# Kernel tuning notes

Hardware: AMD Instinct MI355X
Metric: run time of the kernel (lower is better)

## Reference

```python
import jax, jax.numpy as jnp
import numpy as np

N = 32768      # total nodes (2048 graphs * 16 nodes)
E = 491520     # total edges (2048 graphs * 16*15)
F = 11         # in_node_nf
H = 64         # hidden_nf
G = 2048       # number of graphs
NN = 16        # nodes per graph
R = 1024       # n_reactions
L = 4          # n_layers
EIN = 2 * H + 1        # edge_mlp input: [h[row], h[col], radial]
NIN = H + H + F        # node_mlp input: [h, agg, node_attr=h0]


def setup_inputs() -> dict:
    key = jax.random.key(0)
    ks = jax.random.split(key, 24)
    s = 0.05
    d = {
        "h0": jax.random.normal(ks[0], (N, F), jnp.float32),
        "positions": jax.random.normal(ks[1], (N, 3), jnp.float32),
        "edges": jax.random.randint(ks[2], (2, E), 0, N),
        "node_mask": jnp.ones((N, 1), jnp.float32),
        "edge_mask": jnp.ones((E, 1), jnp.float32),
        "reaction_indexes": jax.random.randint(ks[3], (G,), 0, R),
        "reaction_signs": jax.random.normal(ks[4], (G,), jnp.float32),
        # params
        "emb_w": jax.random.normal(ks[5], (F, H), jnp.float32) * s,
        "emb_b": jnp.zeros((H,), jnp.float32),
        "edge_w1": jax.random.normal(ks[6], (L, EIN, H), jnp.float32) * s,
        "edge_b1": jnp.zeros((L, H), jnp.float32),
        "edge_w2": jax.random.normal(ks[7], (L, H, H), jnp.float32) * s,
        "edge_b2": jnp.zeros((L, H), jnp.float32),
        "node_w1": jax.random.normal(ks[8], (L, NIN, H), jnp.float32) * s,
        "node_b1": jnp.zeros((L, H), jnp.float32),
        "node_w2": jax.random.normal(ks[9], (L, H, H), jnp.float32) * s,
        "node_b2": jnp.zeros((L, H), jnp.float32),
        "dec_w1": jax.random.normal(ks[10], (H, H), jnp.float32) * s,
        "dec_b1": jnp.zeros((H,), jnp.float32),
        "dec_w2": jax.random.normal(ks[11], (H, H), jnp.float32) * s,
        "dec_b2": jnp.zeros((H,), jnp.float32),
        "g_w1": jax.random.normal(ks[12], (H, H), jnp.float32) * s,
        "g_b1": jnp.zeros((H,), jnp.float32),
        "g_w2": jax.random.normal(ks[13], (H, 1), jnp.float32) * s,
        "g_b2": jnp.zeros((1,), jnp.float32),
        "n_nodes": NN,
        "n_reactions": R,
    }
    return d


def reference(h0, positions, edges, node_mask, edge_mask, reaction_indexes,
              reaction_signs, emb_w, emb_b, edge_w1, edge_b1, edge_w2, edge_b2,
              node_w1, node_b1, node_w2, node_b2, dec_w1, dec_b1, dec_w2,
              dec_b2, g_w1, g_b1, g_w2, g_b2, n_nodes, n_reactions):
    silu = jax.nn.silu
    row, col = edges[0], edges[1]
    n = h0.shape[0]

    # radial is constant across layers (coords never updated in this variant)
    coord_diff = positions[row] - positions[col]          # [E, 3]
    radial = jnp.sum(coord_diff ** 2, axis=1, keepdims=True)  # [E, 1]

    h = h0 @ emb_w + emb_b                                # [N, H]
    for i in range(edge_w1.shape[0]):
        # edge model
        e_in = jnp.concatenate([h[row], h[col], radial], axis=1)  # [E, 2H+1]
        e = silu(e_in @ edge_w1[i] + edge_b1[i])
        e = silu(e @ edge_w2[i] + edge_b2[i])             # [E, H]
        e = e * edge_mask
        # scatter-sum aggregation by source node
        agg = jax.ops.segment_sum(e, row, num_segments=n)  # [N, H]
        # node model (node_attr = h0)
        n_in = jnp.concatenate([h, agg, h0], axis=1)      # [N, 2H+F]
        h = silu(n_in @ node_w1[i] + node_b1[i]) @ node_w2[i] + node_b2[i]

    # node decoder
    h = silu(h @ dec_w1 + dec_b1) @ dec_w2 + dec_b2
    h = h * node_mask
    # pool per graph (fixed n_nodes per graph)
    hg = h.reshape(-1, n_nodes, h.shape[-1]).sum(axis=1)  # [G, H]
    # graph decoder
    temp = silu(hg @ g_w1 + g_b1) @ g_w2 + g_b2           # [G, 1]
    # signed per-reaction aggregation
    pred = jnp.zeros((n_reactions,), h.dtype).at[reaction_indexes].add(
        temp[:, 0] * reaction_signs)
    return pred
```

## Files before the change

### kernel.cpp

```cpp
#include <hip/hip_runtime.h>
#include <math.h>

#define N_NODES 32768
#define N_EDGES 491520
#define F_IN    11
#define H       64
#define G_GRAPHS 2048
#define NN_PER_G 16
#define R_REACT 1024
#define L_LAYERS 4
#define EIN     129
#define NIN     139
#define NPBLK   32

typedef __attribute__((ext_vector_type(8))) short short8;
typedef __attribute__((ext_vector_type(4))) float f32x4;

__device__ __forceinline__ float silu_f(float x) {
    return x * __builtin_amdgcn_rcpf(1.0f + __expf(-x));
}
__device__ __forceinline__ void atomAddF(float* p, float v) {
    unsafeAtomicAdd(p, v);
}
__device__ __forceinline__ float bf2f(unsigned short b) {
    union { float f; unsigned u; } v; v.u = ((unsigned)b) << 16;
    return v.f;
}
__device__ __forceinline__ unsigned short f2bf(float x) {
    union { float f; unsigned u; } v; v.f = x;
    unsigned r = v.u + 0x7FFFu + ((v.u >> 16) & 1u);
    return (unsigned short)(r >> 16);
}
__device__ __forceinline__ void splitbf(float x, unsigned short& hi, unsigned short& lo) {
    hi = f2bf(x);
    lo = f2bf(x - bf2f(hi));
}
__device__ __forceinline__ void splitbf_t(float x, unsigned short& hi, unsigned short& lo) {
    union { float f; unsigned u; } v; v.f = x;
    hi = (unsigned short)(v.u >> 16);
    union { float f; unsigned u; } w; w.f = x - bf2f(hi);
    lo = (unsigned short)(w.u >> 16);
}

__global__ __launch_bounds__(256) void k_embed(
        const float* __restrict__ h0, const float* __restrict__ emb_w,
        const float* __restrict__ emb_b, float* __restrict__ h) {
    int tid = blockIdx.x * 256 + threadIdx.x;
    int n = tid >> 6, j = tid & 63;
    float acc = emb_b[j];
#pragma unroll
    for (int k = 0; k < F_IN; ++k)
        acc += h0[n * F_IN + k] * emb_w[k * H + j];
    h[tid] = acc;
}

__global__ __launch_bounds__(256) void k_radial(
        const int* __restrict__ edges, const float* __restrict__ pos,
        float* __restrict__ radial) {
    int e = blockIdx.x * 256 + threadIdx.x;
    int r = edges[e], c = edges[N_EDGES + e];
    float dx = pos[r * 3 + 0] - pos[c * 3 + 0];
    float dy = pos[r * 3 + 1] - pos[c * 3 + 1];
    float dz = pos[r * 3 + 2] - pos[c * 3 + 2];
    radial[e] = dx * dx + dy * dy + dz * dz;
}

__global__ __launch_bounds__(256) void k_hist(
        const int* __restrict__ edges, int* __restrict__ deg) {
    int e = blockIdx.x * 256 + threadIdx.x;
    atomicAdd(&deg[edges[e]], 1);
}

__global__ __launch_bounds__(128) void k_scan_blk(
        const int* __restrict__ deg, int* __restrict__ off,
        int* __restrict__ bsum) {
    __shared__ int sd[128];
    int b = blockIdx.x;
    sd[threadIdx.x] = deg[b * 128 + threadIdx.x];
    __syncthreads();
    if (threadIdx.x == 0) {
        int s = 0;
        for (int i = 0; i < 128; ++i) { int d = sd[i]; sd[i] = s; s += d; }
        bsum[b] = s;
    }
    __syncthreads();
    off[b * 128 + threadIdx.x] = sd[threadIdx.x];
}

__global__ __launch_bounds__(256) void k_scan_top(
        const int* __restrict__ bsum, int* __restrict__ bbase) {
    __shared__ int sb[256];
    sb[threadIdx.x] = bsum[threadIdx.x];
    __syncthreads();
    if (threadIdx.x == 0) {
        int s = 0;
        for (int i = 0; i < 256; ++i) { int d = sb[i]; sb[i] = s; s += d; }
    }
    __syncthreads();
    bbase[threadIdx.x] = sb[threadIdx.x];
}

__global__ __launch_bounds__(256) void k_cursor(
        const int* __restrict__ off, const int* __restrict__ bbase,
        int* __restrict__ nstart, int* __restrict__ cursor) {
    int n = blockIdx.x * 256 + threadIdx.x;
    int ns = off[n] + bbase[n >> 7];
    nstart[n] = ns;
    cursor[n] = ns;
    if (n == 0) nstart[N_NODES] = N_EDGES;
}

__global__ __launch_bounds__(256) void k_fill(
        const int* __restrict__ edges, const float* __restrict__ radial,
        const float* __restrict__ emask, int* __restrict__ cursor,
        int* __restrict__ csrP, float* __restrict__ csrR,
        float* __restrict__ csrM) {
    int e = blockIdx.x * 256 + threadIdx.x;
    int r = edges[e];
    int pos = atomicAdd(&cursor[r], 1);
    csrP[pos] = edges[N_EDGES + e] | ((r & (NPBLK - 1)) << 16);
    csrR[pos] = radial[e];
    csrM[pos] = emask[e];
}

__global__ __launch_bounds__(64, 1) void k_nodeproj_m(
        const float* __restrict__ h, const float* __restrict__ W1,
        const float* __restrict__ b1,
        float* __restrict__ PA, float* __restrict__ PB) {
    const int lane = threadIdx.x;
    const int quad = lane >> 4, m16 = lane & 15;

    short8 Bh[16], Bl[16];
#pragma unroll
    for (int nt = 0; nt < 8; ++nt) {
#pragma unroll
        for (int kf = 0; kf < 2; ++kf) {
            short8 bh, bl;
#pragma unroll
            for (int j = 0; j < 8; ++j) {
                int row = (nt >= 4 ? 64 : 0) + kf * 32 + quad * 8 + j;
                float w = W1[row * H + (nt & 3) * 16 + m16];
                unsigned short hi, lo; splitbf(w, hi, lo);
                bh[j] = (short)hi; bl[j] = (short)lo;
            }
            Bh[nt * 2 + kf] = bh; Bl[nt * 2 + kf] = bl;
        }
    }
    float b1v[4];
#pragma unroll
    for (int nt = 0; nt < 4; ++nt) b1v[nt] = b1[nt * 16 + m16];

    for (int t = 0; t < 2; ++t) {
        const int nb = (blockIdx.x * 2 + t) * 16;
        const float* hp = h + (nb + m16) * H + quad * 8;
        float av[16];
        *(float4*)&av[0]  = *(const float4*)(hp + 0);
        *(float4*)&av[4]  = *(const float4*)(hp + 4);
        *(float4*)&av[8]  = *(const float4*)(hp + 32);
        *(float4*)&av[12] = *(const float4*)(hp + 36);
        short8 Ah0, Ah1, Al0, Al1;
#pragma unroll
        for (int j = 0; j < 8; ++j) {
            unsigned short hi, lo;
            splitbf_t(av[j], hi, lo);     Ah0[j] = (short)hi; Al0[j] = (short)lo;
            splitbf_t(av[8 + j], hi, lo); Ah1[j] = (short)hi; Al1[j] = (short)lo;
        }
        f32x4 acc[8];
#pragma unroll
        for (int nt = 0; nt < 8; ++nt) {
            f32x4 a = {0.0f, 0.0f, 0.0f, 0.0f};
            a = __builtin_amdgcn_mfma_f32_16x16x32_bf16(Ah0, Bh[nt*2+0], a, 0, 0, 0);
            a = __builtin_amdgcn_mfma_f32_16x16x32_bf16(Ah1, Bh[nt*2+1], a, 0, 0, 0);
            a = __builtin_amdgcn_mfma_f32_16x16x32_bf16(Ah0, Bl[nt*2+0], a, 0, 0, 0);
            a = __builtin_amdgcn_mfma_f32_16x16x32_bf16(Ah1, Bl[nt*2+1], a, 0, 0, 0);
            a = __builtin_amdgcn_mfma_f32_16x16x32_bf16(Al0, Bh[nt*2+0], a, 0, 0, 0);
            a = __builtin_amdgcn_mfma_f32_16x16x32_bf16(Al1, Bh[nt*2+1], a, 0, 0, 0);
            acc[nt] = a;
        }
#pragma unroll
        for (int r4 = 0; r4 < 4; ++r4) {
            const int node = nb + quad * 4 + r4;
#pragma unroll
            for (int nt = 0; nt < 4; ++nt)
                PA[node * H + nt * 16 + m16] = acc[nt][r4] + b1v[nt];
#pragma unroll
            for (int nt = 4; nt < 8; ++nt)
                PB[node * H + (nt - 4) * 16 + m16] = acc[nt][r4];
        }
    }
}

__global__ __launch_bounds__(256, 2) void k_edge6(
        const float* __restrict__ PA, const float* __restrict__ PB,
        const int* __restrict__ nstart, const int* __restrict__ csrP,
        const float* __restrict__ csrR, const float* __restrict__ csrM,
        const float* __restrict__ W1,
        const float* __restrict__ W2, const float* __restrict__ b2,
        float* __restrict__ agg) {
    const int tid = threadIdx.x;
    const int lane = tid & 63, wave = tid >> 6;
    const int quad = lane >> 4, m16 = lane & 15;
    const int n0 = blockIdx.x * NPBLK;

    __shared__ float aggld[NPBLK * 68];
    for (int i = tid; i < NPBLK * 68; i += 256) aggld[i] = 0.0f;

    short8 Bh[8], Bl[8];
#pragma unroll
    for (int nt = 0; nt < 4; ++nt) {
#pragma unroll
        for (int kf = 0; kf < 2; ++kf) {
            short8 bh, bl;
#pragma unroll
            for (int j = 0; j < 8; ++j) {
                float w = W2[(kf * 32 + quad * 8 + j) * H + nt * 16 + m16];
                unsigned short hi, lo; splitbf(w, hi, lo);
                bh[j] = (short)hi; bl[j] = (short)lo;
            }
            Bh[nt * 2 + kf] = bh; Bl[nt * 2 + kf] = bl;
        }
    }
    float w1cr[16];
#pragma unroll
    for (int i = 0; i < 16; ++i) {
        int k = (i < 8) ? (quad * 8 + i) : (32 + quad * 8 + (i - 8));
        w1cr[i] = W1[128 * H + k];
    }
    float b2v[4];
#pragma unroll
    for (int nt = 0; nt < 4; ++nt) b2v[nt] = b2[nt * 16 + m16];

    const int start = nstart[n0];
    const int end   = nstart[n0 + NPBLK];
    __syncthreads();

    const int ntiles = (end - start + 15) >> 4;

    float radA = 0.0f, avA[16], bvA[16];
    int rlA = 0;
    int rlqA[4]; float mkqA[4];

    int t = wave;
    bool haveA = t < ntiles;
    if (haveA) {
        const int idx = start + t * 16 + m16;
        const int ss = min(idx, N_EDGES - 1);
        const int pk = csrP[ss];
        radA = csrR[ss];
        const int c = pk & 0xFFFF;
        rlA = pk >> 16;
        const int sb = start + t * 16 + quad * 4;
#pragma unroll
        for (int r4 = 0; r4 < 4; ++r4) {
            int s = sb + r4, s2 = min(s, N_EDGES - 1);
            rlqA[r4] = csrP[s2] >> 16;
            mkqA[r4] = (s < end) ? csrM[s2] : 0.0f;
        }
        const float* par = PA + (n0 + rlA) * H + quad * 8;
        const float* pbr = PB + c * H + quad * 8;
        *(float4*)&avA[0]  = *(const float4*)(par + 0);
        *(float4*)&avA[4]  = *(const float4*)(par + 4);
        *(float4*)&avA[8]  = *(const float4*)(par + 32);
        *(float4*)&avA[12] = *(const float4*)(par + 36);
        *(float4*)&bvA[0]  = *(const float4*)(pbr + 0);
        *(float4*)&bvA[4]  = *(const float4*)(pbr + 4);
        *(float4*)&bvA[8]  = *(const float4*)(pbr + 32);
        *(float4*)&bvA[12] = *(const float4*)(pbr + 36);
    }

    while (haveA) {
        const int tn = t + 4;
        const bool haveB = tn < ntiles;
        float radB = 0.0f, bvB[16];
        int rlB = 0;
        int rlqB[4]; float mkqB[4];
        if (haveB) {
            const int idx = start + tn * 16 + m16;
            const int ss = min(idx, N_EDGES - 1);
            const int pk = csrP[ss];
            radB = csrR[ss];
            const int c = pk & 0xFFFF;
            rlB = pk >> 16;
            const int sb = start + tn * 16 + quad * 4;
#pragma unroll
            for (int r4 = 0; r4 < 4; ++r4) {
                int s = sb + r4, s2 = min(s, N_EDGES - 1);
                rlqB[r4] = csrP[s2] >> 16;
                mkqB[r4] = (s < end) ? csrM[s2] : 0.0f;
            }
            const float* pbr = PB + c * H + quad * 8;
            *(float4*)&bvB[0]  = *(const float4*)(pbr + 0);
            *(float4*)&bvB[4]  = *(const float4*)(pbr + 4);
            *(float4*)&bvB[8]  = *(const float4*)(pbr + 32);
            *(float4*)&bvB[12] = *(const float4*)(pbr + 36);
        }

        short8 Ah0, Ah1, Al0, Al1;
#pragma unroll
        for (int i = 0; i < 8; ++i) {
            unsigned short hi, lo;
            splitbf_t(silu_f(avA[i] + bvA[i] + radA * w1cr[i]), hi, lo);
            Ah0[i] = (short)hi; Al0[i] = (short)lo;
            splitbf_t(silu_f(avA[8+i] + bvA[8+i] + radA * w1cr[8+i]), hi, lo);
            Ah1[i] = (short)hi; Al1[i] = (short)lo;
        }
        f32x4 acc[4];
#pragma unroll
        for (int nt = 0; nt < 4; ++nt) {
            f32x4 a = {0.0f, 0.0f, 0.0f, 0.0f};
            a = __builtin_amdgcn_mfma_f32_16x16x32_bf16(Ah0, Bh[nt*2+0], a, 0, 0, 0);
            a = __builtin_amdgcn_mfma_f32_16x16x32_bf16(Ah1, Bh[nt*2+1], a, 0, 0, 0);
            a = __builtin_amdgcn_mfma_f32_16x16x32_bf16(Ah0, Bl[nt*2+0], a, 0, 0, 0);
            a = __builtin_amdgcn_mfma_f32_16x16x32_bf16(Ah1, Bl[nt*2+1], a, 0, 0, 0);
            a = __builtin_amdgcn_mfma_f32_16x16x32_bf16(Al0, Bh[nt*2+0], a, 0, 0, 0);
            a = __builtin_amdgcn_mfma_f32_16x16x32_bf16(Al1, Bh[nt*2+1], a, 0, 0, 0);
            acc[nt] = a;
        }

#pragma unroll
        for (int nt = 0; nt < 4; ++nt) {
            float oo[4];
#pragma unroll
            for (int r4 = 0; r4 < 4; ++r4)
                oo[r4] = silu_f(acc[nt][r4] + b2v[nt]) * mkqA[r4];
            int cur = rlqA[0]; float s = oo[0];
#pragma unroll
            for (int r4 = 1; r4 < 4; ++r4) {
                if (rlqA[r4] == cur) { s += oo[r4]; }
                else {
                    atomicAdd(&aggld[cur * 68 + nt * 16 + m16], s);
                    cur = rlqA[r4]; s = oo[r4];
                }
            }
            atomicAdd(&aggld[cur * 68 + nt * 16 + m16], s);
        }

        if (haveB) {
            radA = radB; rlA = rlB;
#pragma unroll
            for (int r4 = 0; r4 < 4; ++r4) { rlqA[r4] = rlqB[r4]; mkqA[r4] = mkqB[r4]; }
            const float* par = PA + (n0 + rlA) * H + quad * 8;
            *(float4*)&avA[0]  = *(const float4*)(par + 0);
            *(float4*)&avA[4]  = *(const float4*)(par + 4);
            *(float4*)&avA[8]  = *(const float4*)(par + 32);
            *(float4*)&avA[12] = *(const float4*)(par + 36);
#pragma unroll
            for (int i = 0; i < 16; ++i) bvA[i] = bvB[i];
        }
        t = tn; haveA = haveB;
    }

    __syncthreads();
#pragma unroll
    for (int i = tid; i < NPBLK * 16; i += 256) {
        int n = i >> 4, cb = (i & 15) << 2;
        *(float4*)&agg[(n0 + n) * H + cb] = *(const float4*)&aggld[n * 68 + cb];
    }
}

__global__ __launch_bounds__(64, 1) void k_node_m(
        float* __restrict__ h, const float* __restrict__ agg,
        const float* __restrict__ h0,
        const float* __restrict__ W1, const float* __restrict__ b1,
        const float* __restrict__ W2, const float* __restrict__ b2) {
    const int lane = threadIdx.x;
    const int quad = lane >> 4, m16 = lane & 15;

    short8 B1h[20], B1l[20];
#pragma unroll
    for (int nt = 0; nt < 4; ++nt) {
#pragma unroll
        for (int kf = 0; kf < 5; ++kf) {
            short8 bh, bl;
#pragma unroll
            for (int j = 0; j < 8; ++j) {
                int row = kf * 32 + quad * 8 + j;
                float w = (row < NIN) ? W1[row * H + nt * 16 + m16] : 0.0f;
                unsigned short hi, lo; splitbf(w, hi, lo);
                bh[j] = (short)hi; bl[j] = (short)lo;
            }
            B1h[nt * 5 + kf] = bh; B1l[nt * 5 + kf] = bl;
        }
    }
    short8 B2h[8], B2l[8];
#pragma unroll
    for (int nt = 0; nt < 4; ++nt) {
#pragma unroll
        for (int kf = 0; kf < 2; ++kf) {
            short8 bh, bl;
#pragma unroll
            for (int j = 0; j < 8; ++j) {
                float w = W2[(kf * 32 + quad * 8 + j) * H + nt * 16 + m16];
                unsigned short hi, lo; splitbf(w, hi, lo);
                bh[j] = (short)hi; bl[j] = (short)lo;
            }
            B2h[nt * 2 + kf] = bh; B2l[nt * 2 + kf] = bl;
        }
    }
    float b1v[4], b2v[4];
#pragma unroll
    for (int nt = 0; nt < 4; ++nt) {
        b1v[nt] = b1[nt * 16 + m16];
        b2v[nt] = b2[nt * 16 + m16];
    }

    __shared__ float tld[16 * 68];

    for (int t = 0; t < 2; ++t) {
        const int nb = (blockIdx.x * 2 + t) * 16;
        float a1[5][8];
        const float* hp = h + (nb + m16) * H + quad * 8;
        const float* ap = agg + (nb + m16) * H + quad * 8;
        *(float4*)&a1[0][0] = *(const float4*)(hp + 0);
        *(float4*)&a1[0][4] = *(const float4*)(hp + 4);
        *(float4*)&a1[1][0] = *(const float4*)(hp + 32);
        *(float4*)&a1[1][4] = *(const float4*)(hp + 36);
        *(float4*)&a1[2][0] = *(const float4*)(ap + 0);
        *(float4*)&a1[2][4] = *(const float4*)(ap + 4);
        *(float4*)&a1[3][0] = *(const float4*)(ap + 32);
        *(float4*)&a1[3][4] = *(const float4*)(ap + 36);
        const float* h0p = h0 + (nb + m16) * F_IN;
#pragma unroll
        for (int j = 0; j < 8; ++j) {
            int kk = quad * 8 + j;
            a1[4][j] = (kk < F_IN) ? h0p[kk] : 0.0f;
        }
        short8 A1h[5], A1l[5];
#pragma unroll
        for (int kf = 0; kf < 5; ++kf) {
            short8 ah, al;
#pragma unroll
            for (int j = 0; j < 8; ++j) {
                unsigned short hi, lo; splitbf_t(a1[kf][j], hi, lo);
                ah[j] = (short)hi; al[j] = (short)lo;
            }
            A1h[kf] = ah; A1l[kf] = al;
        }
        f32x4 acc[4];
#pragma unroll
        for (int nt = 0; nt < 4; ++nt) {
            f32x4 a = {0.0f, 0.0f, 0.0f, 0.0f};
#pragma unroll
            for (int kf = 0; kf < 5; ++kf)
                a = __builtin_amdgcn_mfma_f32_16x16x32_bf16(A1h[kf], B1h[nt*5+kf], a, 0, 0, 0);
#pragma unroll
            for (int kf = 0; kf < 5; ++kf)
                a = __builtin_amdgcn_mfma_f32_16x16x32_bf16(A1h[kf], B1l[nt*5+kf], a, 0, 0, 0);
#pragma unroll
            for (int kf = 0; kf < 5; ++kf)
                a = __builtin_amdgcn_mfma_f32_16x16x32_bf16(A1l[kf], B1h[nt*5+kf], a, 0, 0, 0);
            acc[nt] = a;
        }
#pragma unroll
        for (int r4 = 0; r4 < 4; ++r4)
#pragma unroll
            for (int nt = 0; nt < 4; ++nt)
                tld[(quad * 4 + r4) * 68 + nt * 16 + m16] =
                    silu_f(acc[nt][r4] + b1v[nt]);
        __syncthreads();
        float a2[16];
        *(float4*)&a2[0]  = *(const float4*)&tld[m16 * 68 + quad * 8 + 0];
        *(float4*)&a2[4]  = *(const float4*)&tld[m16 * 68 + quad * 8 + 4];
        *(float4*)&a2[8]  = *(const float4*)&tld[m16 * 68 + quad * 8 + 32];
        *(float4*)&a2[12] = *(const float4*)&tld[m16 * 68 + quad * 8 + 36];
        short8 A2h0, A2h1, A2l0, A2l1;
#pragma unroll
        for (int j = 0; j < 8; ++j) {
            unsigned short hi, lo;
            splitbf_t(a2[j], hi, lo);     A2h0[j] = (short)hi; A2l0[j] = (short)lo;
            splitbf_t(a2[8+j], hi, lo);   A2h1[j] = (short)hi; A2l1[j] = (short)lo;
        }
        f32x4 acc2[4];
#pragma unroll
        for (int nt = 0; nt < 4; ++nt) {
            f32x4 a = {0.0f, 0.0f, 0.0f, 0.0f};
            a = __builtin_amdgcn_mfma_f32_16x16x32_bf16(A2h0, B2h[nt*2+0], a, 0, 0, 0);
            a = __builtin_amdgcn_mfma_f32_16x16x32_bf16(A2h1, B2h[nt*2+1], a, 0, 0, 0);
            a = __builtin_amdgcn_mfma_f32_16x16x32_bf16(A2h0, B2l[nt*2+0], a, 0, 0, 0);
            a = __builtin_amdgcn_mfma_f32_16x16x32_bf16(A2h1, B2l[nt*2+1], a, 0, 0, 0);
            a = __builtin_amdgcn_mfma_f32_16x16x32_bf16(A2l0, B2h[nt*2+0], a, 0, 0, 0);
            a = __builtin_amdgcn_mfma_f32_16x16x32_bf16(A2l1, B2h[nt*2+1], a, 0, 0, 0);
            acc2[nt] = a;
        }
#pragma unroll
        for (int r4 = 0; r4 < 4; ++r4) {
            const int node = nb + quad * 4 + r4;
#pragma unroll
            for (int nt = 0; nt < 4; ++nt)
                h[node * H + nt * 16 + m16] = acc2[nt][r4] + b2v[nt];
        }
        __syncthreads();
    }
}

__global__ __launch_bounds__(64, 1) void k_dec_m(
        float* __restrict__ h, const float* __restrict__ nmask,
        const float* __restrict__ W1, const float* __restrict__ b1,
        const float* __restrict__ W2, const float* __restrict__ b2) {
    const int lane = threadIdx.x;
    const int quad = lane >> 4, m16 = lane & 15;

    short8 B1h[8], B1l[8], B2h[8], B2l[8];
#pragma unroll
    for (int nt = 0; nt < 4; ++nt) {
#pragma unroll
        for (int kf = 0; kf < 2; ++kf) {
            short8 bh1, bl1, bh2, bl2;
#pragma unroll
            for (int j = 0; j < 8; ++j) {
                int row = kf * 32 + quad * 8 + j;
                unsigned short hi, lo;
                splitbf(W1[row * H + nt * 16 + m16], hi, lo);
                bh1[j] = (short)hi; bl1[j] = (short)lo;
                splitbf(W2[row * H + nt * 16 + m16], hi, lo);
                bh2[j] = (short)hi; bl2[j] = (short)lo;
            }
            B1h[nt*2+kf] = bh1; B1l[nt*2+kf] = bl1;
            B2h[nt*2+kf] = bh2; B2l[nt*2+kf] = bl2;
        }
    }
    float b1v[4], b2v[4];
#pragma unroll
    for (int nt = 0; nt < 4; ++nt) {
        b1v[nt] = b1[nt * 16 + m16];
        b2v[nt] = b2[nt * 16 + m16];
    }
    __shared__ float tld[16 * 68];

    for (int t = 0; t < 2; ++t) {
        const int nb = (blockIdx.x * 2 + t) * 16;
        const float* hp = h + (nb + m16) * H + quad * 8;
        float av[16];
        *(float4*)&av[0]  = *(const float4*)(hp + 0);
        *(float4*)&av[4]  = *(const float4*)(hp + 4);
        *(float4*)&av[8]  = *(const float4*)(hp + 32);
        *(float4*)&av[12] = *(const float4*)(hp + 36);
        short8 Ah0, Ah1, Al0, Al1;
#pragma unroll
        for (int j = 0; j < 8; ++j) {
            unsigned short hi, lo;
            splitbf_t(av[j], hi, lo);     Ah0[j] = (short)hi; Al0[j] = (short)lo;
            splitbf_t(av[8+j], hi, lo);   Ah1[j] = (short)hi; Al1[j] = (short)lo;
        }
        f32x4 acc[4];
#pragma unroll
        for (int nt = 0; nt < 4; ++nt) {
            f32x4 a = {0.0f, 0.0f, 0.0f, 0.0f};
            a = __builtin_amdgcn_mfma_f32_16x16x32_bf16(Ah0, B1h[nt*2+0], a, 0, 0, 0);
            a = __builtin_amdgcn_mfma_f32_16x16x32_bf16(Ah1, B1h[nt*2+1], a, 0, 0, 0);
            a = __builtin_amdgcn_mfma_f32_16x16x32_bf16(Ah0, B1l[nt*2+0], a, 0, 0, 0);
            a = __builtin_amdgcn_mfma_f32_16x16x32_bf16(Ah1, B1l[nt*2+1], a, 0, 0, 0);
            a = __builtin_amdgcn_mfma_f32_16x16x32_bf16(Al0, B1h[nt*2+0], a, 0, 0, 0);
            a = __builtin_amdgcn_mfma_f32_16x16x32_bf16(Al1, B1h[nt*2+1], a, 0, 0, 0);
            acc[nt] = a;
        }
#pragma unroll
        for (int r4 = 0; r4 < 4; ++r4)
#pragma unroll
            for (int nt = 0; nt < 4; ++nt)
                tld[(quad * 4 + r4) * 68 + nt * 16 + m16] =
                    silu_f(acc[nt][r4] + b1v[nt]);
        __syncthreads();
        float a2[16];
        *(float4*)&a2[0]  = *(const float4*)&tld[m16 * 68 + quad * 8 + 0];
        *(float4*)&a2[4]  = *(const float4*)&tld[m16 * 68 + quad * 8 + 4];
        *(float4*)&a2[8]  = *(const float4*)&tld[m16 * 68 + quad * 8 + 32];
        *(float4*)&a2[12] = *(const float4*)&tld[m16 * 68 + quad * 8 + 36];
        short8 A2h0, A2h1, A2l0, A2l1;
#pragma unroll
        for (int j = 0; j < 8; ++j) {
            unsigned short hi, lo;
            splitbf_t(a2[j], hi, lo);     A2h0[j] = (short)hi; A2l0[j] = (short)lo;
            splitbf_t(a2[8+j], hi, lo);   A2h1[j] = (short)hi; A2l1[j] = (short)lo;
        }
        f32x4 acc2[4];
#pragma unroll
        for (int nt = 0; nt < 4; ++nt) {
            f32x4 a = {0.0f, 0.0f, 0.0f, 0.0f};
            a = __builtin_amdgcn_mfma_f32_16x16x32_bf16(A2h0, B2h[nt*2+0], a, 0, 0, 0);
            a = __builtin_amdgcn_mfma_f32_16x16x32_bf16(A2h1, B2h[nt*2+1], a, 0, 0, 0);
            a = __builtin_amdgcn_mfma_f32_16x16x32_bf16(A2h0, B2l[nt*2+0], a, 0, 0, 0);
            a = __builtin_amdgcn_mfma_f32_16x16x32_bf16(A2h1, B2l[nt*2+1], a, 0, 0, 0);
            a = __builtin_amdgcn_mfma_f32_16x16x32_bf16(A2l0, B2h[nt*2+0], a, 0, 0, 0);
            a = __builtin_amdgcn_mfma_f32_16x16x32_bf16(A2l1, B2h[nt*2+1], a, 0, 0, 0);
            acc2[nt] = a;
        }
#pragma unroll
        for (int r4 = 0; r4 < 4; ++r4) {
            const int node = nb + quad * 4 + r4;
            const float nm = nmask[node];
#pragma unroll
            for (int nt = 0; nt < 4; ++nt)
                h[node * H + nt * 16 + m16] = (acc2[nt][r4] + b2v[nt]) * nm;
        }
        __syncthreads();
    }
}

__global__ __launch_bounds__(64) void k_graph(
        const float* __restrict__ h, const int* __restrict__ rid,
        const float* __restrict__ rsign,
        const float* __restrict__ W1, const float* __restrict__ b1,
        const float* __restrict__ W2, const float* __restrict__ b2,
        float* __restrict__ pred) {
    const int g = blockIdx.x;
    const int lane = threadIdx.x;
    float hgv = 0.0f;
#pragma unroll
    for (int m = 0; m < NN_PER_G; ++m)
        hgv += h[(g * NN_PER_G + m) * H + lane];
    __shared__ __align__(16) float hgs[64];
    hgs[lane] = hgv;
    __syncthreads();
    float acc = b1[lane];
#pragma unroll
    for (int k = 0; k < H; ++k)
        acc += hgs[k] * W1[k * H + lane];
    float part = silu_f(acc) * W2[lane];
#pragma unroll
    for (int off = 32; off > 0; off >>= 1)
        part += __shfl_down(part, off);
    if (lane == 0)
        atomAddF(&pred[rid[g]], (part + b2[0]) * rsign[g]);
}

extern "C" void kernel_launch(void* const* d_in, const int* in_sizes, int n_in,
                              void* d_out, int out_size, void* d_ws, size_t ws_size,
                              hipStream_t stream) {
    const float* h0      = (const float*)d_in[0];
    const float* pos     = (const float*)d_in[1];
    const int*   edges   = (const int*)d_in[2];
    const float* nmask   = (const float*)d_in[3];
    const float* emask   = (const float*)d_in[4];
    const int*   rid     = (const int*)d_in[5];
    const float* rsign   = (const float*)d_in[6];
    const float* emb_w   = (const float*)d_in[7];
    const float* emb_b   = (const float*)d_in[8];
    const float* edge_w1 = (const float*)d_in[9];
    const float* edge_b1 = (const float*)d_in[10];
    const float* edge_w2 = (const float*)d_in[11];
    const float* edge_b2 = (const float*)d_in[12];
    const float* node_w1 = (const float*)d_in[13];
    const float* node_b1 = (const float*)d_in[14];
    const float* node_w2 = (const float*)d_in[15];
    const float* node_b2 = (const float*)d_in[16];
    const float* dec_w1  = (const float*)d_in[17];
    const float* dec_b1  = (const float*)d_in[18];
    const float* dec_w2  = (const float*)d_in[19];
    const float* dec_b2  = (const float*)d_in[20];
    const float* g_w1    = (const float*)d_in[21];
    const float* g_b1    = (const float*)d_in[22];
    const float* g_w2    = (const float*)d_in[23];
    const float* g_b2    = (const float*)d_in[24];

    float* h      = (float*)d_ws;
    float* agg    = h + N_NODES * H;
    float* radial = agg + N_NODES * H;
    float* PA     = radial + N_EDGES;
    float* PB     = PA + N_NODES * H;
    float* csrR   = PB + N_NODES * H;
    float* csrM   = csrR + N_EDGES;
    int*   csrP   = (int*)(csrM + N_EDGES);
    int*   deg    = csrP + N_EDGES;
    int*   off    = deg + N_NODES;
    int*   bsum   = off + N_NODES;
    int*   bbase  = bsum + 256;
    int*   nstart = bbase + 256;
    int*   cursor = nstart + N_NODES + 1;
    float* pred   = (float*)d_out;

    hipMemsetAsync(d_out, 0, R_REACT * sizeof(float), stream);
    hipMemsetAsync(deg, 0, N_NODES * sizeof(int), stream);

    k_embed<<<(N_NODES * H) / 256, 256, 0, stream>>>(h0, emb_w, emb_b, h);
    k_radial<<<N_EDGES / 256, 256, 0, stream>>>(edges, pos, radial);
    k_hist<<<N_EDGES / 256, 256, 0, stream>>>(edges, deg);
    k_scan_blk<<<256, 128, 0, stream>>>(deg, off, bsum);
    k_scan_top<<<1, 256, 0, stream>>>(bsum, bbase);
    k_cursor<<<N_NODES / 256, 256, 0, stream>>>(off, bbase, nstart, cursor);
    k_fill<<<N_EDGES / 256, 256, 0, stream>>>(edges, radial, emask, cursor,
                                              csrP, csrR, csrM);

    for (int i = 0; i < L_LAYERS; ++i) {
        k_nodeproj_m<<<N_NODES / 32, 64, 0, stream>>>(
            h, edge_w1 + i * EIN * H, edge_b1 + i * H, PA, PB);
        k_edge6<<<N_NODES / NPBLK, 256, 0, stream>>>(
            PA, PB, nstart, csrP, csrR, csrM,
            edge_w1 + i * EIN * H,
            edge_w2 + i * H * H, edge_b2 + i * H, agg);
        k_node_m<<<N_NODES / 32, 64, 0, stream>>>(
            h, agg, h0,
            node_w1 + i * NIN * H, node_b1 + i * H,
            node_w2 + i * H * H,   node_b2 + i * H);
    }
    k_dec_m<<<N_NODES / 32, 64, 0, stream>>>(h, nmask, dec_w1, dec_b1,
                                             dec_w2, dec_b2);
    k_graph<<<G_GRAPHS, 64, 0, stream>>>(h, rid, rsign, g_w1, g_b1, g_w2,
                                         g_b2, pred);
}
```

Measured before the change: 561.2 us.

## Stage split-bf16 weights in shared memory and use 4-wave blocks for node MLP kernels

```diff
diff --git a/kernel.cpp b/kernel.cpp
--- a/kernel.cpp
+++ b/kernel.cpp
@@ -123,35 +123,30 @@
     csrM[pos] = emask[e];
 }
 
-__global__ __launch_bounds__(64, 1) void k_nodeproj_m(
+#define KP_P 136
+__global__ __launch_bounds__(256, 2) void k_nodeproj_m(
         const float* __restrict__ h, const float* __restrict__ W1,
         const float* __restrict__ b1,
         float* __restrict__ PA, float* __restrict__ PB) {
-    const int lane = threadIdx.x;
+    const int tid = threadIdx.x;
+    const int lane = tid & 63, wave = tid >> 6;
     const int quad = lane >> 4, m16 = lane & 15;
 
-    short8 Bh[16], Bl[16];
-#pragma unroll
-    for (int nt = 0; nt < 8; ++nt) {
-#pragma unroll
-        for (int kf = 0; kf < 2; ++kf) {
-            short8 bh, bl;
-#pragma unroll
-            for (int j = 0; j < 8; ++j) {
-                int row = (nt >= 4 ? 64 : 0) + kf * 32 + quad * 8 + j;
-                float w = W1[row * H + (nt & 3) * 16 + m16];
-                unsigned short hi, lo; splitbf(w, hi, lo);
-                bh[j] = (short)hi; bl[j] = (short)lo;
-            }
-            Bh[nt * 2 + kf] = bh; Bl[nt * 2 + kf] = bl;
-        }
+    __shared__ unsigned short Whi[64 * KP_P], Wlo[64 * KP_P];
+    for (int i = tid; i < 64 * KP_P; i += 256) {
+        int k = i >> 6, n = i & 63;
+        float w = (k < 128) ? W1[k * H + n] : 0.0f;
+        unsigned short hi, lo; splitbf(w, hi, lo);
+        Whi[n * KP_P + k] = hi;
+        Wlo[n * KP_P + k] = lo;
     }
     float b1v[4];
 #pragma unroll
     for (int nt = 0; nt < 4; ++nt) b1v[nt] = b1[nt * 16 + m16];
+    __syncthreads();
 
     for (int t = 0; t < 2; ++t) {
-        const int nb = (blockIdx.x * 2 + t) * 16;
+        const int nb = (blockIdx.x * 8 + wave * 2 + t) * 16;
         const float* hp = h + (nb + m16) * H + quad * 8;
         float av[16];
         *(float4*)&av[0]  = *(const float4*)(hp + 0);
@@ -168,13 +163,21 @@
         f32x4 acc[8];
 #pragma unroll
         for (int nt = 0; nt < 8; ++nt) {
+            const int col = (nt & 3) * 16 + m16;
+            const int kb  = (nt >= 4 ? 64 : 0) + quad * 8;
+            const unsigned short* ch = &Whi[col * KP_P + kb];
+            const unsigned short* cl = &Wlo[col * KP_P + kb];
             f32x4 a = {0.0f, 0.0f, 0.0f, 0.0f};
-            a = __builtin_amdgcn_mfma_f32_16x16x32_bf16(Ah0, Bh[nt*2+0], a, 0, 0, 0);
-            a = __builtin_amdgcn_mfma_f32_16x16x32_bf16(Ah1, Bh[nt*2+1], a, 0, 0, 0);
-            a = __builtin_amdgcn_mfma_f32_16x16x32_bf16(Ah0, Bl[nt*2+0], a, 0, 0, 0);
-            a = __builtin_amdgcn_mfma_f32_16x16x32_bf16(Ah1, Bl[nt*2+1], a, 0, 0, 0);
-            a = __builtin_amdgcn_mfma_f32_16x16x32_bf16(Al0, Bh[nt*2+0], a, 0, 0, 0);
-            a = __builtin_amdgcn_mfma_f32_16x16x32_bf16(Al1, Bh[nt*2+1], a, 0, 0, 0);
+            short8 bh0 = *(const short8*)(ch +  0);
+            short8 bh1 = *(const short8*)(ch + 32);
+            short8 bl0 = *(const short8*)(cl +  0);
+            short8 bl1 = *(const short8*)(cl + 32);
+            a = __builtin_amdgcn_mfma_f32_16x16x32_bf16(Ah0, bh0, a, 0, 0, 0);
+            a = __builtin_amdgcn_mfma_f32_16x16x32_bf16(Ah1, bh1, a, 0, 0, 0);
+            a = __builtin_amdgcn_mfma_f32_16x16x32_bf16(Ah0, bl0, a, 0, 0, 0);
+            a = __builtin_amdgcn_mfma_f32_16x16x32_bf16(Ah1, bl1, a, 0, 0, 0);
+            a = __builtin_amdgcn_mfma_f32_16x16x32_bf16(Al0, bh0, a, 0, 0, 0);
+            a = __builtin_amdgcn_mfma_f32_16x16x32_bf16(Al1, bh1, a, 0, 0, 0);
             acc[nt] = a;
         }
 #pragma unroll
@@ -358,44 +361,34 @@
     }
 }
 
-__global__ __launch_bounds__(64, 1) void k_node_m(
+#define KP_N 168
+#define KP_2 72
+__global__ __launch_bounds__(256, 2) void k_node_m(
         float* __restrict__ h, const float* __restrict__ agg,
         const float* __restrict__ h0,
         const float* __restrict__ W1, const float* __restrict__ b1,
         const float* __restrict__ W2, const float* __restrict__ b2) {
-    const int lane = threadIdx.x;
+    const int tid = threadIdx.x;
+    const int lane = tid & 63, wave = tid >> 6;
     const int quad = lane >> 4, m16 = lane & 15;
 
-    short8 B1h[20], B1l[20];
-#pragma unroll
-    for (int nt = 0; nt < 4; ++nt) {
-#pragma unroll
-        for (int kf = 0; kf < 5; ++kf) {
-            short8 bh, bl;
-#pragma unroll
-            for (int j = 0; j < 8; ++j) {
-                int row = kf * 32 + quad * 8 + j;
-                float w = (row < NIN) ? W1[row * H + nt * 16 + m16] : 0.0f;
-                unsigned short hi, lo; splitbf(w, hi, lo);
-                bh[j] = (short)hi; bl[j] = (short)lo;
-            }
-            B1h[nt * 5 + kf] = bh; B1l[nt * 5 + kf] = bl;
-        }
-    }
-    short8 B2h[8], B2l[8];
-#pragma unroll
-    for (int nt = 0; nt < 4; ++nt) {
-#pragma unroll
-        for (int kf = 0; kf < 2; ++kf) {
-            short8 bh, bl;
-#pragma unroll
-            for (int j = 0; j < 8; ++j) {
-                float w = W2[(kf * 32 + quad * 8 + j) * H + nt * 16 + m16];
-                unsigned short hi, lo; splitbf(w, hi, lo);
-                bh[j] = (short)hi; bl[j] = (short)lo;
-            }
-            B2h[nt * 2 + kf] = bh; B2l[nt * 2 + kf] = bl;
-        }
+    __shared__ unsigned short W1h[64 * KP_N], W1l[64 * KP_N];
+    __shared__ unsigned short W2h[64 * KP_2], W2l[64 * KP_2];
+    __shared__ float tld[4][16 * 68];
+
+    for (int i = tid; i < 64 * KP_N; i += 256) {
+        int k = i >> 6, n = i & 63;
+        float w = (k < NIN) ? W1[k * H + n] : 0.0f;
+        unsigned short hi, lo; splitbf(w, hi, lo);
+        W1h[n * KP_N + k] = hi;
+        W1l[n * KP_N + k] = lo;
+    }
+    for (int i = tid; i < 64 * KP_2; i += 256) {
+        int k = i >> 6, n = i & 63;
+        float w = (k < H) ? W2[k * H + n] : 0.0f;
+        unsigned short hi, lo; splitbf(w, hi, lo);
+        W2h[n * KP_2 + k] = hi;
+        W2l[n * KP_2 + k] = lo;
     }
     float b1v[4], b2v[4];
 #pragma unroll
@@ -403,11 +396,10 @@
         b1v[nt] = b1[nt * 16 + m16];
         b2v[nt] = b2[nt * 16 + m16];
     }
-
-    __shared__ float tld[16 * 68];
+    __syncthreads();
 
     for (int t = 0; t < 2; ++t) {
-        const int nb = (blockIdx.x * 2 + t) * 16;
+        const int nb = (blockIdx.x * 8 + wave * 2 + t) * 16;
         float a1[5][8];
         const float* hp = h + (nb + m16) * H + quad * 8;
         const float* ap = agg + (nb + m16) * H + quad * 8;
@@ -439,30 +431,31 @@
         f32x4 acc[4];
 #pragma unroll
         for (int nt = 0; nt < 4; ++nt) {
+            const unsigned short* ch = &W1h[(nt * 16 + m16) * KP_N + quad * 8];
+            const unsigned short* cl = &W1l[(nt * 16 + m16) * KP_N + quad * 8];
             f32x4 a = {0.0f, 0.0f, 0.0f, 0.0f};
 #pragma unroll
-            for (int kf = 0; kf < 5; ++kf)
-                a = __builtin_amdgcn_mfma_f32_16x16x32_bf16(A1h[kf], B1h[nt*5+kf], a, 0, 0, 0);
-#pragma unroll
-            for (int kf = 0; kf < 5; ++kf)
-                a = __builtin_amdgcn_mfma_f32_16x16x32_bf16(A1h[kf], B1l[nt*5+kf], a, 0, 0, 0);
-#pragma unroll
-            for (int kf = 0; kf < 5; ++kf)
-                a = __builtin_amdgcn_mfma_f32_16x16x32_bf16(A1l[kf], B1h[nt*5+kf], a, 0, 0, 0);
+            for (int kf = 0; kf < 5; ++kf) {
+                short8 bh = *(const short8*)(ch + kf * 32);
+                short8 bl = *(const short8*)(cl + kf * 32);
+                a = __builtin_amdgcn_mfma_f32_16x16x32_bf16(A1h[kf], bh, a, 0, 0, 0);
+                a = __builtin_amdgcn_mfma_f32_16x16x32_bf16(A1l[kf], bh, a, 0, 0, 0);
+                a = __builtin_amdgcn_mfma_f32_16x16x32_bf16(A1h[kf], bl, a, 0, 0, 0);
+            }
             acc[nt] = a;
         }
 #pragma unroll
         for (int r4 = 0; r4 < 4; ++r4)
 #pragma unroll
             for (int nt = 0; nt < 4; ++nt)
-                tld[(quad * 4 + r4) * 68 + nt * 16 + m16] =
+                tld[wave][(quad * 4 + r4) * 68 + nt * 16 + m16] =
                     silu_f(acc[nt][r4] + b1v[nt]);
         __syncthreads();
         float a2[16];
-        *(float4*)&a2[0]  = *(const float4*)&tld[m16 * 68 + quad * 8 + 0];
-        *(float4*)&a2[4]  = *(const float4*)&tld[m16 * 68 + quad * 8 + 4];
-        *(float4*)&a2[8]  = *(const float4*)&tld[m16 * 68 + quad * 8 + 32];
-        *(float4*)&a2[12] = *(const float4*)&tld[m16 * 68 + quad * 8 + 36];
+        *(float4*)&a2[0]  = *(const float4*)&tld[wave][m16 * 68 + quad * 8 + 0];
+        *(float4*)&a2[4]  = *(const float4*)&tld[wave][m16 * 68 + quad * 8 + 4];
+        *(float4*)&a2[8]  = *(const float4*)&tld[wave][m16 * 68 + quad * 8 + 32];
+        *(float4*)&a2[12] = *(const float4*)&tld[wave][m16 * 68 + quad * 8 + 36];
         short8 A2h0, A2h1, A2l0, A2l1;
 #pragma unroll
         for (int j = 0; j < 8; ++j) {
@@ -473,13 +466,19 @@
         f32x4 acc2[4];
 #pragma unroll
         for (int nt = 0; nt < 4; ++nt) {
+            const unsigned short* ch = &W2h[(nt * 16 + m16) * KP_2 + quad * 8];
+            const unsigned short* cl = &W2l[(nt * 16 + m16) * KP_2 + quad * 8];
             f32x4 a = {0.0f, 0.0f, 0.0f, 0.0f};
-            a = __builtin_amdgcn_mfma_f32_16x16x32_bf16(A2h0, B2h[nt*2+0], a, 0, 0, 0);
-            a = __builtin_amdgcn_mfma_f32_16x16x32_bf16(A2h1, B2h[nt*2+1], a, 0, 0, 0);
-            a = __builtin_amdgcn_mfma_f32_16x16x32_bf16(A2h0, B2l[nt*2+0], a, 0, 0, 0);
-            a = __builtin_amdgcn_mfma_f32_16x16x32_bf16(A2h1, B2l[nt*2+1], a, 0, 0, 0);
-            a = __builtin_amdgcn_mfma_f32_16x16x32_bf16(A2l0, B2h[nt*2+0], a, 0, 0, 0);
-            a = __builtin_amdgcn_mfma_f32_16x16x32_bf16(A2l1, B2h[nt*2+1], a, 0, 0, 0);
+            short8 bh0 = *(const short8*)(ch +  0);
+            short8 bh1 = *(const short8*)(ch + 32);
+            short8 bl0 = *(const short8*)(cl +  0);
+            short8 bl1 = *(const short8*)(cl + 32);
+            a = __builtin_amdgcn_mfma_f32_16x16x32_bf16(A2h0, bh0, a, 0, 0, 0);
+            a = __builtin_amdgcn_mfma_f32_16x16x32_bf16(A2h1, bh1, a, 0, 0, 0);
+            a = __builtin_amdgcn_mfma_f32_16x16x32_bf16(A2h0, bl0, a, 0, 0, 0);
+            a = __builtin_amdgcn_mfma_f32_16x16x32_bf16(A2h1, bl1, a, 0, 0, 0);
+            a = __builtin_amdgcn_mfma_f32_16x16x32_bf16(A2l0, bh0, a, 0, 0, 0);
+            a = __builtin_amdgcn_mfma_f32_16x16x32_bf16(A2l1, bh1, a, 0, 0, 0);
             acc2[nt] = a;
         }
 #pragma unroll
@@ -493,31 +492,27 @@
     }
 }
 
-__global__ __launch_bounds__(64, 1) void k_dec_m(
+__global__ __launch_bounds__(256, 2) void k_dec_m(
         float* __restrict__ h, const float* __restrict__ nmask,
         const float* __restrict__ W1, const float* __restrict__ b1,
         const float* __restrict__ W2, const float* __restrict__ b2) {
-    const int lane = threadIdx.x;
+    const int tid = threadIdx.x;
+    const int lane = tid & 63, wave = tid >> 6;
     const int quad = lane >> 4, m16 = lane & 15;
 
-    short8 B1h[8], B1l[8], B2h[8], B2l[8];
-#pragma unroll
-    for (int nt = 0; nt < 4; ++nt) {
-#pragma unroll
-        for (int kf = 0; kf < 2; ++kf) {
-            short8 bh1, bl1, bh2, bl2;
-#pragma unroll
-            for (int j = 0; j < 8; ++j) {
-                int row = kf * 32 + quad * 8 + j;
-                unsigned short hi, lo;
-                splitbf(W1[row * H + nt * 16 + m16], hi, lo);
-                bh1[j] = (short)hi; bl1[j] = (short)lo;
-                splitbf(W2[row * H + nt * 16 + m16], hi, lo);
-                bh2[j] = (short)hi; bl2[j] = (short)lo;
-            }
-            B1h[nt*2+kf] = bh1; B1l[nt*2+kf] = bl1;
-            B2h[nt*2+kf] = bh2; B2l[nt*2+kf] = bl2;
-        }
+    __shared__ unsigned short W1h[64 * KP_2], W1l[64 * KP_2];
+    __shared__ unsigned short W2h[64 * KP_2], W2l[64 * KP_2];
+    __shared__ float tld[4][16 * 68];
+
+    for (int i = tid; i < 64 * KP_2; i += 256) {
+        int k = i >> 6, n = i & 63;
+        unsigned short hi, lo;
+        float w1 = (k < H) ? W1[k * H + n] : 0.0f;
+        splitbf(w1, hi, lo);
+        W1h[n * KP_2 + k] = hi; W1l[n * KP_2 + k] = lo;
+        float w2 = (k < H) ? W2[k * H + n] : 0.0f;
+        splitbf(w2, hi, lo);
+        W2h[n * KP_2 + k] = hi; W2l[n * KP_2 + k] = lo;
     }
     float b1v[4], b2v[4];
 #pragma unroll
@@ -525,10 +520,10 @@
         b1v[nt] = b1[nt * 16 + m16];
         b2v[nt] = b2[nt * 16 + m16];
     }
-    __shared__ float tld[16 * 68];
+    __syncthreads();
 
     for (int t = 0; t < 2; ++t) {
-        const int nb = (blockIdx.x * 2 + t) * 16;
+        const int nb = (blockIdx.x * 8 + wave * 2 + t) * 16;
         const float* hp = h + (nb + m16) * H + quad * 8;
         float av[16];
         *(float4*)&av[0]  = *(const float4*)(hp + 0);
@@ -545,27 +540,33 @@
         f32x4 acc[4];
 #pragma unroll
         for (int nt = 0; nt < 4; ++nt) {
+            const unsigned short* ch = &W1h[(nt * 16 + m16) * KP_2 + quad * 8];
+            const unsigned short* cl = &W1l[(nt * 16 + m16) * KP_2 + quad * 8];
             f32x4 a = {0.0f, 0.0f, 0.0f, 0.0f};
-            a = __builtin_amdgcn_mfma_f32_16x16x32_bf16(Ah0, B1h[nt*2+0], a, 0, 0, 0);
-            a = __builtin_amdgcn_mfma_f32_16x16x32_bf16(Ah1, B1h[nt*2+1], a, 0, 0, 0);
-            a = __builtin_amdgcn_mfma_f32_16x16x32_bf16(Ah0, B1l[nt*2+0], a, 0, 0, 0);
-            a = __builtin_amdgcn_mfma_f32_16x16x32_bf16(Ah1, B1l[nt*2+1], a, 0, 0, 0);
-            a = __builtin_amdgcn_mfma_f32_16x16x32_bf16(Al0, B1h[nt*2+0], a, 0, 0, 0);
-            a = __builtin_amdgcn_mfma_f32_16x16x32_bf16(Al1, B1h[nt*2+1], a, 0, 0, 0);
+            short8 bh0 = *(const short8*)(ch +  0);
+            short8 bh1 = *(const short8*)(ch + 32);
+            short8 bl0 = *(const short8*)(cl +  0);
+            short8 bl1 = *(const short8*)(cl + 32);
+            a = __builtin_amdgcn_mfma_f32_16x16x32_bf16(Ah0, bh0, a, 0, 0, 0);
+            a = __builtin_amdgcn_mfma_f32_16x16x32_bf16(Ah1, bh1, a, 0, 0, 0);
+            a = __builtin_amdgcn_mfma_f32_16x16x32_bf16(Ah0, bl0, a, 0, 0, 0);
+            a = __builtin_amdgcn_mfma_f32_16x16x32_bf16(Ah1, bl1, a, 0, 0, 0);
+            a = __builtin_amdgcn_mfma_f32_16x16x32_bf16(Al0, bh0, a, 0, 0, 0);
+            a = __builtin_amdgcn_mfma_f32_16x16x32_bf16(Al1, bh1, a, 0, 0, 0);
             acc[nt] = a;
         }
 #pragma unroll
         for (int r4 = 0; r4 < 4; ++r4)
 #pragma unroll
             for (int nt = 0; nt < 4; ++nt)
-                tld[(quad * 4 + r4) * 68 + nt * 16 + m16] =
+                tld[wave][(quad * 4 + r4) * 68 + nt * 16 + m16] =
                     silu_f(acc[nt][r4] + b1v[nt]);
         __syncthreads();
         float a2[16];
-        *(float4*)&a2[0]  = *(const float4*)&tld[m16 * 68 + quad * 8 + 0];
-        *(float4*)&a2[4]  = *(const float4*)&tld[m16 * 68 + quad * 8 + 4];
-        *(float4*)&a2[8]  = *(const float4*)&tld[m16 * 68 + quad * 8 + 32];
-        *(float4*)&a2[12] = *(const float4*)&tld[m16 * 68 + quad * 8 + 36];
+        *(float4*)&a2[0]  = *(const float4*)&tld[wave][m16 * 68 + quad * 8 + 0];
+        *(float4*)&a2[4]  = *(const float4*)&tld[wave][m16 * 68 + quad * 8 + 4];
+        *(float4*)&a2[8]  = *(const float4*)&tld[wave][m16 * 68 + quad * 8 + 32];
+        *(float4*)&a2[12] = *(const float4*)&tld[wave][m16 * 68 + quad * 8 + 36];
         short8 A2h0, A2h1, A2l0, A2l1;
 #pragma unroll
         for (int j = 0; j < 8; ++j) {
@@ -576,13 +577,19 @@
         f32x4 acc2[4];
 #pragma unroll
         for (int nt = 0; nt < 4; ++nt) {
+            const unsigned short* ch = &W2h[(nt * 16 + m16) * KP_2 + quad * 8];
+            const unsigned short* cl = &W2l[(nt * 16 + m16) * KP_2 + quad * 8];
             f32x4 a = {0.0f, 0.0f, 0.0f, 0.0f};
-            a = __builtin_amdgcn_mfma_f32_16x16x32_bf16(A2h0, B2h[nt*2+0], a, 0, 0, 0);
-            a = __builtin_amdgcn_mfma_f32_16x16x32_bf16(A2h1, B2h[nt*2+1], a, 0, 0, 0);
-            a = __builtin_amdgcn_mfma_f32_16x16x32_bf16(A2h0, B2l[nt*2+0], a, 0, 0, 0);
-            a = __builtin_amdgcn_mfma_f32_16x16x32_bf16(A2h1, B2l[nt*2+1], a, 0, 0, 0);
-            a = __builtin_amdgcn_mfma_f32_16x16x32_bf16(A2l0, B2h[nt*2+0], a, 0, 0, 0);
-            a = __builtin_amdgcn_mfma_f32_16x16x32_bf16(A2l1, B2h[nt*2+1], a, 0, 0, 0);
+            short8 bh0 = *(const short8*)(ch +  0);
+            short8 bh1 = *(const short8*)(ch + 32);
+            short8 bl0 = *(const short8*)(cl +  0);
+            short8 bl1 = *(const short8*)(cl + 32);
+            a = __builtin_amdgcn_mfma_f32_16x16x32_bf16(A2h0, bh0, a, 0, 0, 0);
+            a = __builtin_amdgcn_mfma_f32_16x16x32_bf16(A2h1, bh1, a, 0, 0, 0);
+            a = __builtin_amdgcn_mfma_f32_16x16x32_bf16(A2h0, bl0, a, 0, 0, 0);
+            a = __builtin_amdgcn_mfma_f32_16x16x32_bf16(A2h1, bl1, a, 0, 0, 0);
+            a = __builtin_amdgcn_mfma_f32_16x16x32_bf16(A2l0, bh0, a, 0, 0, 0);
+            a = __builtin_amdgcn_mfma_f32_16x16x32_bf16(A2l1, bh1, a, 0, 0, 0);
             acc2[nt] = a;
         }
 #pragma unroll
@@ -682,19 +689,19 @@
                                               csrP, csrR, csrM);
 
     for (int i = 0; i < L_LAYERS; ++i) {
-        k_nodeproj_m<<<N_NODES / 32, 64, 0, stream>>>(
+        k_nodeproj_m<<<N_NODES / 128, 256, 0, stream>>>(
             h, edge_w1 + i * EIN * H, edge_b1 + i * H, PA, PB);
         k_edge6<<<N_NODES / NPBLK, 256, 0, stream>>>(
             PA, PB, nstart, csrP, csrR, csrM,
             edge_w1 + i * EIN * H,
             edge_w2 + i * H * H, edge_b2 + i * H, agg);
-        k_node_m<<<N_NODES / 32, 64, 0, stream>>>(
+        k_node_m<<<N_NODES / 128, 256, 0, stream>>>(
             h, agg, h0,
             node_w1 + i * NIN * H, node_b1 + i * H,
             node_w2 + i * H * H,   node_b2 + i * H);
     }
-    k_dec_m<<<N_NODES / 32, 64, 0, stream>>>(h, nmask, dec_w1, dec_b1,
-                                             dec_w2, dec_b2);
+    k_dec_m<<<N_NODES / 128, 256, 0, stream>>>(h, nmask, dec_w1, dec_b1,
+                                               dec_w2, dec_b2);
     k_graph<<<G_GRAPHS, 64, 0, stream>>>(h, rid, rsign, g_w1, g_b1, g_w2,
                                          g_b2, pred);
 }
```

New measurement: 633.8 us. 12.9% more time.
